# Kernel optimization log

Hardware: AMD Instinct MI355X
Metric: run time of the kernel (lower is better)

Reference implementation:

```python
import math
import jax, jax.numpy as jnp
import numpy as np

B, A, U, S, E, HYP, H = 16384, 32, 64, 2048, 32, 64, 4
ATTEND_REG_COEF = 1e-3


def setup_inputs() -> dict:
    key = jax.random.key(0)
    ks = jax.random.split(key, 12)
    sc = 0.05
    return {
        "agent_qs": jax.random.normal(ks[0], (B, A), jnp.float32),
        "states": jax.random.normal(ks[1], (B, S), jnp.float32),
        # per-head selector hypernet: Linear(S,HYP)+ReLU+Linear(HYP,E,no bias)
        "sel_w1": jax.random.normal(ks[2], (H, S, HYP), jnp.float32) * sc,
        "sel_b1": jax.random.normal(ks[3], (H, HYP), jnp.float32) * sc,
        "sel_w2": jax.random.normal(ks[4], (H, HYP, E), jnp.float32) * sc,
        # per-head key extractor: Linear(U,E,no bias)
        "key_w": jax.random.normal(ks[5], (H, U, E), jnp.float32) * sc,
        # V net: Linear(S,E)+ReLU+Linear(E,1)
        "v_w1": jax.random.normal(ks[6], (S, E), jnp.float32) * sc,
        "v_b1": jax.random.normal(ks[7], (E,), jnp.float32) * sc,
        "v_w2": jax.random.normal(ks[8], (E, 1), jnp.float32) * sc,
        "v_b2": jax.random.normal(ks[9], (1,), jnp.float32) * sc,
    }


def reference(agent_qs, states, sel_w1, sel_b1, sel_w2, key_w, v_w1, v_b1, v_w2, v_b2):
    # nonlinear=False, weighted_head=False, state_bias=True (defaults used here)
    unit_states = states[:, : A * U].reshape(-1, A, U)  # [B, A, U]

    # per-head selectors: [B, H, E]
    h1 = jax.nn.relu(jnp.einsum("bs,hsk->bhk", states, sel_w1) + sel_b1[None])
    selectors = jnp.einsum("bhk,hke->bhe", h1, sel_w2)

    # per-head, per-agent keys: [B, H, A, E]
    keys = jnp.einsum("bau,hue->bhae", unit_states, key_w)

    # attention logits [B, H, A] (matches selector @ stacked-keys in torch)
    logits = jnp.einsum("bhe,bhae->bha", selectors, keys)
    weights = jax.nn.softmax(logits / math.sqrt(E), axis=-1)  # [B, H, A]

    head_attend = jnp.sum(weights, axis=1)  # [B, A]

    v = jax.nn.relu(states @ v_w1 + v_b1) @ v_w2 + v_b2  # [B, 1]

    # coef * sum over heads of mean(logits_h ** 2)
    attend_mag_regs = ATTEND_REG_COEF * jnp.sum(jnp.mean(logits ** 2, axis=(0, 2)))

    # per-head entropy: -(p * log(p + 1e-8)).sum(agents).mean(batch) -> [H]
    head_entropies = -jnp.mean(
        jnp.sum(weights * jnp.log(weights + 1e-8), axis=-1), axis=0
    )

    return head_attend, v, attend_mag_regs, head_entropies
```

## Files before the change

### kernel.cpp

```cpp
#include <hip/hip_runtime.h>
#include <hip/hip_bf16.h>

#define B_N 16384
#define A_N 32
#define U_N 64
#define S_N 2048
#define E_N 32
#define HYP_N 64
#define H_N 4
#define NPAD 320
#define NREAL 288

#define WS_SB    0
#define WS_WT    67108864
#define WS_C1    (67108864 + 1310720)
#define WS_KWT   (WS_C1 + 9437184)
#define WS_PMAG  (WS_KWT + 32768)
#define WS_PENT  (WS_PMAG + 65536)

#define OUT_V   (B_N * A_N)
#define OUT_MAG (OUT_V + B_N)
#define OUT_ENT (OUT_MAG + 1)

typedef __attribute__((ext_vector_type(8))) short bf16x8_t;
typedef __attribute__((ext_vector_type(4))) float floatx4_t;

#define AS1(p) ((const __attribute__((address_space(1))) void*)(p))
#define AS3(p) ((__attribute__((address_space(3))) void*)(p))

__device__ __forceinline__ unsigned short f2b(float f) {
    union { float f; unsigned u; } v; v.f = f;
    unsigned r = v.u + 0x7FFFu + ((v.u >> 16) & 1u);
    return (unsigned short)(r >> 16);
}
__device__ __forceinline__ float b2f(unsigned x) {
    union { unsigned u; float f; } v; v.u = x << 16; return v.f;
}

__global__ __launch_bounds__(256) void cvt_states_kernel(
        const float* __restrict__ in, unsigned short* __restrict__ outp) {
    size_t i = ((size_t)blockIdx.x * 256 + threadIdx.x) * 8;
    float4 a = *(const float4*)(in + i);
    float4 b = *(const float4*)(in + i + 4);
    uint4 o;
    o.x = (unsigned)f2b(a.x) | ((unsigned)f2b(a.y) << 16);
    o.y = (unsigned)f2b(a.z) | ((unsigned)f2b(a.w) << 16);
    o.z = (unsigned)f2b(b.x) | ((unsigned)f2b(b.y) << 16);
    o.w = (unsigned)f2b(b.z) | ((unsigned)f2b(b.w) << 16);
    *(uint4*)(outp + i) = o;
}

__global__ __launch_bounds__(256) void pack_w_kernel(
        const float* __restrict__ sel_w1, const float* __restrict__ v_w1,
        const float* __restrict__ key_w,
        unsigned short* __restrict__ Wt, float* __restrict__ kwT) {
    int idx = blockIdx.x * 256 + threadIdx.x;
    if (idx < NPAD * S_N) {
        int n = idx >> 11;
        int k = idx & 2047;
        float val = 0.0f;
        if (n < 256) {
            int h = n >> 6, kk = n & 63;
            val = sel_w1[((size_t)h * S_N + k) * HYP_N + kk];
        } else if (n < NREAL) {
            val = v_w1[(size_t)k * E_N + (n - 256)];
        }
        Wt[idx] = f2b(val);
    } else if (idx < NPAD * S_N + H_N * E_N * U_N) {
        int j = idx - NPAD * S_N;
        int h = j >> 11, e = (j >> 6) & 31, u = j & 63;
        kwT[j] = key_w[((size_t)h * U_N + u) * E_N + e];
    }
}

#define GM_BM 128
#define GM_BN 64
#define GM_BK 64

__global__ __launch_bounds__(256) void gemm1_mfma_kernel(
        const unsigned short* __restrict__ Sb, const unsigned short* __restrict__ Wt,
        const float* __restrict__ sel_b1, const float* __restrict__ v_b1,
        unsigned short* __restrict__ C1) {
    __shared__ __align__(16) unsigned short Asm[GM_BM * GM_BK];
    __shared__ __align__(16) unsigned short Bsm[GM_BN * GM_BK];

    const int t = threadIdx.x;
    const int lane = t & 63;
    const int w = t >> 6;
    const int m0 = blockIdx.y * GM_BM;
    const int n0 = blockIdx.x * GM_BN;
    const int mw = (w >> 1) * 64;
    const int nw = (w & 1) * 32;

    floatx4_t acc[4][2] = {};

    for (int k0 = 0; k0 < S_N; k0 += GM_BK) {
        __syncthreads();
#pragma unroll
        for (int i = 0; i < 4; ++i) {
            int p = i * 256 + t;
            int r = p >> 3;
            int cl = (p & 7) ^ (r & 7);
            const unsigned short* g = Sb + (size_t)(m0 + r) * S_N + k0 + cl * 8;
            __builtin_amdgcn_global_load_lds(AS1(g), AS3(Asm + p * 8), 16, 0, 0);
        }
#pragma unroll
        for (int i = 0; i < 2; ++i) {
            int p = i * 256 + t;
            int n = p >> 3;
            int cl = (p & 7) ^ (n & 7);
            const unsigned short* g = Wt + (size_t)(n0 + n) * S_N + k0 + cl * 8;
            __builtin_amdgcn_global_load_lds(AS1(g), AS3(Bsm + p * 8), 16, 0, 0);
        }
        __syncthreads();

#pragma unroll
        for (int s = 0; s < 2; ++s) {
            const int c = s * 4 + (lane >> 4);
            bf16x8_t bfr[2];
#pragma unroll
            for (int nt = 0; nt < 2; ++nt) {
                int n = nw + nt * 16 + (lane & 15);
                int ph = c ^ (n & 7);
                bfr[nt] = *(const bf16x8_t*)(Bsm + n * 64 + ph * 8);
            }
#pragma unroll
            for (int mt = 0; mt < 4; ++mt) {
                int r = mw + mt * 16 + (lane & 15);
                int ph = c ^ (r & 7);
                bf16x8_t afr = *(const bf16x8_t*)(Asm + r * 64 + ph * 8);
#pragma unroll
                for (int nt = 0; nt < 2; ++nt)
                    acc[mt][nt] = __builtin_amdgcn_mfma_f32_16x16x32_bf16(
                        afr, bfr[nt], acc[mt][nt], 0, 0, 0);
            }
        }
    }

#pragma unroll
    for (int nt = 0; nt < 2; ++nt) {
        int n = n0 + nw + nt * 16 + (lane & 15);
        if (n >= NREAL) continue;
        float bias = (n < 256) ? sel_b1[n] : v_b1[n - 256];
#pragma unroll
        for (int mt = 0; mt < 4; ++mt) {
            int rbase = m0 + mw + mt * 16 + (lane >> 4) * 4;
#pragma unroll
            for (int rg = 0; rg < 4; ++rg) {
                float v = acc[mt][nt][rg] + bias;
                C1[(size_t)(rbase + rg) * NREAL + n] = f2b(v > 0.0f ? v : 0.0f);
            }
        }
    }
}

__global__ __launch_bounds__(256) void epilogue2_kernel(
        const unsigned short* __restrict__ Sb, const unsigned short* __restrict__ C1,
        const float* __restrict__ sel_w2, const float* __restrict__ kwT,
        const float* __restrict__ v_w2, const float* __restrict__ v_b2,
        float* __restrict__ out, float* __restrict__ pmag, float* __restrict__ pent) {
    __shared__ float us[4][A_N * 65];
    __shared__ float h1s[4][NREAL];
    __shared__ float sel_s[4][H_N * E_N];
    __shared__ float ts[4][H_N * U_N];

    const int t = threadIdx.x;
    const int w = t >> 6;
    const int lane = t & 63;
    const int b = blockIdx.x * 4 + w;

#pragma unroll
    for (int i = 0; i < 4; ++i) {
        int c = i * 64 + lane;
        uint4 v = *(const uint4*)(Sb + (size_t)b * S_N + c * 8);
        int a = c >> 3, u0 = (c & 7) * 8;
        float* d = &us[w][a * 65 + u0];
        d[0] = b2f(v.x & 0xffff); d[1] = b2f(v.x >> 16);
        d[2] = b2f(v.y & 0xffff); d[3] = b2f(v.y >> 16);
        d[4] = b2f(v.z & 0xffff); d[5] = b2f(v.z >> 16);
        d[6] = b2f(v.w & 0xffff); d[7] = b2f(v.w >> 16);
    }
    if (lane < 36) {
        uint4 v = *(const uint4*)(C1 + (size_t)b * NREAL + lane * 8);
        float* d = &h1s[w][lane * 8];
        d[0] = b2f(v.x & 0xffff); d[1] = b2f(v.x >> 16);
        d[2] = b2f(v.y & 0xffff); d[3] = b2f(v.y >> 16);
        d[4] = b2f(v.z & 0xffff); d[5] = b2f(v.z >> 16);
        d[6] = b2f(v.w & 0xffff); d[7] = b2f(v.w >> 16);
    }
    __syncthreads();

#pragma unroll
    for (int l = 0; l < 2; ++l) {
        int idx = l * 64 + lane, h = idx >> 5, e = idx & 31;
        const float* hh = &h1s[w][h * HYP_N];
        const float* w2 = sel_w2 + (size_t)h * HYP_N * E_N + e;
        float s = 0.0f;
#pragma unroll
        for (int k = 0; k < HYP_N; ++k) s = fmaf(hh[k], w2[(size_t)k * E_N], s);
        sel_s[w][idx] = s;
    }
    __syncthreads();

#pragma unroll
    for (int l = 0; l < 4; ++l) {
        int idx = l * 64 + lane, h = idx >> 6, u = idx & 63;
        const float* sh = &sel_s[w][h * E_N];
        const float* kw = kwT + (size_t)h * E_N * U_N + u;
        float s = 0.0f;
#pragma unroll
        for (int e = 0; e < E_N; ++e) s = fmaf(sh[e], kw[(size_t)e * U_N], s);
        ts[w][idx] = s;
    }
    __syncthreads();

    float wgt[2];
    float mag = 0.0f;
#pragma unroll
    for (int l = 0; l < 2; ++l) {
        int idx = l * 64 + lane, h = idx >> 5, a = idx & 31;
        const float* ua = &us[w][a * 65];
        const float* th = &ts[w][h * U_N];
        float lg = 0.0f;
#pragma unroll
        for (int u = 0; u < U_N; ++u) lg = fmaf(ua[u], th[u], lg);
        mag += lg * lg;

        float x = lg * 0.17677669529663687f;
        float m = x;
#pragma unroll
        for (int o = 16; o > 0; o >>= 1) m = fmaxf(m, __shfl_xor(m, o, 32));
        float p = expf(x - m);
        float den = p;
#pragma unroll
        for (int o = 16; o > 0; o >>= 1) den += __shfl_xor(den, o, 32);
        float wv = p / den;
        wgt[l] = wv;

        float ent = wv * logf(wv + 1e-8f);
#pragma unroll
        for (int o = 16; o > 0; o >>= 1) ent += __shfl_xor(ent, o, 32);
        if (a == 0) pent[(size_t)h * B_N + b] = ent;
    }

#pragma unroll
    for (int o = 32; o > 0; o >>= 1) mag += __shfl_xor(mag, o, 64);
    if (lane == 0) pmag[b] = mag;

    float partial = wgt[0] + wgt[1];
    partial += __shfl_xor(partial, 32, 64);
    if (lane < 32) out[(size_t)b * A_N + lane] = partial;

    if (lane < 32) {
        float p = h1s[w][256 + lane] * v_w2[lane];
#pragma unroll
        for (int o = 16; o > 0; o >>= 1) p += __shfl_xor(p, o, 32);
        if (lane == 0) out[OUT_V + b] = p + v_b2[0];
    }
}

__global__ __launch_bounds__(256) void finalize_kernel(
        const float* __restrict__ pmag, const float* __restrict__ pent,
        float* __restrict__ out) {
    int which = blockIdx.x;
    const float* src = (which == 0) ? pmag : (pent + (size_t)(which - 1) * B_N);
    float s = 0.0f;
    for (int i = threadIdx.x; i < B_N; i += 256) s += src[i];
#pragma unroll
    for (int o = 32; o > 0; o >>= 1) s += __shfl_xor(s, o, 64);
    __shared__ float red[4];
    if ((threadIdx.x & 63) == 0) red[threadIdx.x >> 6] = s;
    __syncthreads();
    if (threadIdx.x == 0) {
        float tot = red[0] + red[1] + red[2] + red[3];
        if (which == 0) out[OUT_MAG] = 1e-3f * tot / (float)(B_N * A_N);
        else out[OUT_ENT + which - 1] = -tot / (float)B_N;
    }
}

extern "C" void kernel_launch(void* const* d_in, const int* in_sizes, int n_in,
                              void* d_out, int out_size, void* d_ws, size_t ws_size,
                              hipStream_t stream) {
    const float* states = (const float*)d_in[1];
    const float* sel_w1 = (const float*)d_in[2];
    const float* sel_b1 = (const float*)d_in[3];
    const float* sel_w2 = (const float*)d_in[4];
    const float* key_w  = (const float*)d_in[5];
    const float* v_w1   = (const float*)d_in[6];
    const float* v_b1   = (const float*)d_in[7];
    const float* v_w2   = (const float*)d_in[8];
    const float* v_b2   = (const float*)d_in[9];
    float* out = (float*)d_out;
    char* wsb  = (char*)d_ws;

    unsigned short* Sb  = (unsigned short*)(wsb + WS_SB);
    unsigned short* Wt  = (unsigned short*)(wsb + WS_WT);
    unsigned short* C1  = (unsigned short*)(wsb + WS_C1);
    float* kwT          = (float*)(wsb + WS_KWT);
    float* pmag         = (float*)(wsb + WS_PMAG);
    float* pent         = (float*)(wsb + WS_PENT);

    cvt_states_kernel<<<dim3(B_N * S_N / (256 * 8)), dim3(256), 0, stream>>>(states, Sb);
    pack_w_kernel<<<dim3((NPAD * S_N + H_N * E_N * U_N + 255) / 256), dim3(256), 0, stream>>>(
        sel_w1, v_w1, key_w, Wt, kwT);
    gemm1_mfma_kernel<<<dim3(NPAD / GM_BN, B_N / GM_BM), dim3(256), 0, stream>>>(
        Sb, Wt, sel_b1, v_b1, C1);
    epilogue2_kernel<<<dim3(B_N / 4), dim3(256), 0, stream>>>(
        Sb, C1, sel_w2, kwT, v_w2, v_b2, out, pmag, pent);
    finalize_kernel<<<dim3(5), dim3(256), 0, stream>>>(pmag, pent, out);
}
```

Measured before the change: 340.6 us.

## Fuse states fp32-to-bf16 conversion into GEMM and cover full N per block

Removes the separate states conversion kernel and its 64MB bf16 intermediate. The GEMM now loads fp32 states directly, converts them to bf16 in registers and stores them into swizzled LDS. Each block computes all 288 output columns for 64 rows, so states are read only once instead of once per N-tile, and the padding to 320 columns is dropped. The epilogue reads fp32 states directly. The trade-off is a larger LDS footprint, more accumulator registers per block, and synchronous loads of A that are no longer asynchronous LDS loads.

```diff
diff --git a/kernel.cpp b/kernel.cpp
--- a/kernel.cpp
+++ b/kernel.cpp
@@ -8,12 +8,10 @@
 #define E_N 32
 #define HYP_N 64
 #define H_N 4
-#define NPAD 320
 #define NREAL 288
 
-#define WS_SB    0
-#define WS_WT    67108864
-#define WS_C1    (67108864 + 1310720)
+#define WS_WT    0
+#define WS_C1    1179648
 #define WS_KWT   (WS_C1 + 9437184)
 #define WS_PMAG  (WS_KWT + 32768)
 #define WS_PENT  (WS_PMAG + 65536)
@@ -35,19 +33,6 @@
 }
 __device__ __forceinline__ float b2f(unsigned x) {
     union { unsigned u; float f; } v; v.u = x << 16; return v.f;
-}
-
-__global__ __launch_bounds__(256) void cvt_states_kernel(
-        const float* __restrict__ in, unsigned short* __restrict__ outp) {
-    size_t i = ((size_t)blockIdx.x * 256 + threadIdx.x) * 8;
-    float4 a = *(const float4*)(in + i);
-    float4 b = *(const float4*)(in + i + 4);
-    uint4 o;
-    o.x = (unsigned)f2b(a.x) | ((unsigned)f2b(a.y) << 16);
-    o.y = (unsigned)f2b(a.z) | ((unsigned)f2b(a.w) << 16);
-    o.z = (unsigned)f2b(b.x) | ((unsigned)f2b(b.y) << 16);
-    o.w = (unsigned)f2b(b.z) | ((unsigned)f2b(b.w) << 16);
-    *(uint4*)(outp + i) = o;
 }
 
 __global__ __launch_bounds__(256) void pack_w_kernel(
@@ -55,95 +40,103 @@
         const float* __restrict__ key_w,
         unsigned short* __restrict__ Wt, float* __restrict__ kwT) {
     int idx = blockIdx.x * 256 + threadIdx.x;
-    if (idx < NPAD * S_N) {
+    if (idx < NREAL * S_N) {
         int n = idx >> 11;
         int k = idx & 2047;
-        float val = 0.0f;
+        float val;
         if (n < 256) {
             int h = n >> 6, kk = n & 63;
             val = sel_w1[((size_t)h * S_N + k) * HYP_N + kk];
-        } else if (n < NREAL) {
+        } else {
             val = v_w1[(size_t)k * E_N + (n - 256)];
         }
         Wt[idx] = f2b(val);
-    } else if (idx < NPAD * S_N + H_N * E_N * U_N) {
-        int j = idx - NPAD * S_N;
+    } else if (idx < NREAL * S_N + H_N * E_N * U_N) {
+        int j = idx - NREAL * S_N;
         int h = j >> 11, e = (j >> 6) & 31, u = j & 63;
         kwT[j] = key_w[((size_t)h * U_N + u) * E_N + e];
     }
 }
 
-#define GM_BM 128
-#define GM_BN 64
+#define GM_BM 64
 #define GM_BK 64
 
-__global__ __launch_bounds__(256) void gemm1_mfma_kernel(
-        const unsigned short* __restrict__ Sb, const unsigned short* __restrict__ Wt,
+__global__ __launch_bounds__(256) void gemm2_kernel(
+        const float* __restrict__ states, const unsigned short* __restrict__ Wt,
         const float* __restrict__ sel_b1, const float* __restrict__ v_b1,
         unsigned short* __restrict__ C1) {
     __shared__ __align__(16) unsigned short Asm[GM_BM * GM_BK];
-    __shared__ __align__(16) unsigned short Bsm[GM_BN * GM_BK];
+    __shared__ __align__(16) unsigned short Bsm[NREAL * GM_BK];
 
     const int t = threadIdx.x;
     const int lane = t & 63;
     const int w = t >> 6;
-    const int m0 = blockIdx.y * GM_BM;
-    const int n0 = blockIdx.x * GM_BN;
-    const int mw = (w >> 1) * 64;
-    const int nw = (w & 1) * 32;
-
-    floatx4_t acc[4][2] = {};
+    const int m0 = blockIdx.x * GM_BM;
+    const int mw = (w >> 1) * 32;
+    const int nw = (w & 1) * 144;
+
+    floatx4_t acc[2][9] = {};
 
     for (int k0 = 0; k0 < S_N; k0 += GM_BK) {
         __syncthreads();
-#pragma unroll
-        for (int i = 0; i < 4; ++i) {
-            int p = i * 256 + t;
-            int r = p >> 3;
-            int cl = (p & 7) ^ (r & 7);
-            const unsigned short* g = Sb + (size_t)(m0 + r) * S_N + k0 + cl * 8;
-            __builtin_amdgcn_global_load_lds(AS1(g), AS3(Asm + p * 8), 16, 0, 0);
-        }
+
+        float4 av[2][2];
 #pragma unroll
         for (int i = 0; i < 2; ++i) {
-            int p = i * 256 + t;
-            int n = p >> 3;
-            int cl = (p & 7) ^ (n & 7);
-            const unsigned short* g = Wt + (size_t)(n0 + n) * S_N + k0 + cl * 8;
+            int p = i * 256 + t, r = p >> 3, cl = p & 7;
+            const float* g = states + (size_t)(m0 + r) * S_N + k0 + cl * 8;
+            av[i][0] = *(const float4*)g;
+            av[i][1] = *(const float4*)(g + 4);
+        }
+#pragma unroll
+        for (int i = 0; i < 9; ++i) {
+            int p = i * 256 + t, n = p >> 3, sl = p & 7;
+            int cl = sl ^ (n & 7);
+            const unsigned short* g = Wt + (size_t)n * S_N + k0 + cl * 8;
             __builtin_amdgcn_global_load_lds(AS1(g), AS3(Bsm + p * 8), 16, 0, 0);
+        }
+#pragma unroll
+        for (int i = 0; i < 2; ++i) {
+            int p = i * 256 + t, r = p >> 3, cl = p & 7;
+            int ph = cl ^ (r & 7);
+            uint4 o;
+            o.x = (unsigned)f2b(av[i][0].x) | ((unsigned)f2b(av[i][0].y) << 16);
+            o.y = (unsigned)f2b(av[i][0].z) | ((unsigned)f2b(av[i][0].w) << 16);
+            o.z = (unsigned)f2b(av[i][1].x) | ((unsigned)f2b(av[i][1].y) << 16);
+            o.w = (unsigned)f2b(av[i][1].z) | ((unsigned)f2b(av[i][1].w) << 16);
+            *(uint4*)(Asm + (size_t)(r * 8 + ph) * 8) = o;
         }
         __syncthreads();
 
 #pragma unroll
         for (int s = 0; s < 2; ++s) {
             const int c = s * 4 + (lane >> 4);
-            bf16x8_t bfr[2];
-#pragma unroll
-            for (int nt = 0; nt < 2; ++nt) {
+            bf16x8_t afr[2];
+#pragma unroll
+            for (int mt = 0; mt < 2; ++mt) {
+                int r = mw + mt * 16 + (lane & 15);
+                int ph = c ^ (r & 7);
+                afr[mt] = *(const bf16x8_t*)(Asm + r * 64 + ph * 8);
+            }
+#pragma unroll
+            for (int nt = 0; nt < 9; ++nt) {
                 int n = nw + nt * 16 + (lane & 15);
                 int ph = c ^ (n & 7);
-                bfr[nt] = *(const bf16x8_t*)(Bsm + n * 64 + ph * 8);
+                bf16x8_t bfr = *(const bf16x8_t*)(Bsm + n * 64 + ph * 8);
+                acc[0][nt] = __builtin_amdgcn_mfma_f32_16x16x32_bf16(
+                    afr[0], bfr, acc[0][nt], 0, 0, 0);
+                acc[1][nt] = __builtin_amdgcn_mfma_f32_16x16x32_bf16(
+                    afr[1], bfr, acc[1][nt], 0, 0, 0);
             }
-#pragma unroll
-            for (int mt = 0; mt < 4; ++mt) {
-                int r = mw + mt * 16 + (lane & 15);
-                int ph = c ^ (r & 7);
-                bf16x8_t afr = *(const bf16x8_t*)(Asm + r * 64 + ph * 8);
-#pragma unroll
-                for (int nt = 0; nt < 2; ++nt)
-                    acc[mt][nt] = __builtin_amdgcn_mfma_f32_16x16x32_bf16(
-                        afr, bfr[nt], acc[mt][nt], 0, 0, 0);
-            }
-        }
-    }
-
-#pragma unroll
-    for (int nt = 0; nt < 2; ++nt) {
-        int n = n0 + nw + nt * 16 + (lane & 15);
-        if (n >= NREAL) continue;
+        }
+    }
+
+#pragma unroll
+    for (int nt = 0; nt < 9; ++nt) {
+        int n = nw + nt * 16 + (lane & 15);
         float bias = (n < 256) ? sel_b1[n] : v_b1[n - 256];
 #pragma unroll
-        for (int mt = 0; mt < 4; ++mt) {
+        for (int mt = 0; mt < 2; ++mt) {
             int rbase = m0 + mw + mt * 16 + (lane >> 4) * 4;
 #pragma unroll
             for (int rg = 0; rg < 4; ++rg) {
@@ -155,7 +148,7 @@
 }
 
 __global__ __launch_bounds__(256) void epilogue2_kernel(
-        const unsigned short* __restrict__ Sb, const unsigned short* __restrict__ C1,
+        const float* __restrict__ states, const unsigned short* __restrict__ C1,
         const float* __restrict__ sel_w2, const float* __restrict__ kwT,
         const float* __restrict__ v_w2, const float* __restrict__ v_b2,
         float* __restrict__ out, float* __restrict__ pmag, float* __restrict__ pent) {
@@ -169,16 +162,16 @@
     const int lane = t & 63;
     const int b = blockIdx.x * 4 + w;
 
-#pragma unroll
-    for (int i = 0; i < 4; ++i) {
-        int c = i * 64 + lane;
-        uint4 v = *(const uint4*)(Sb + (size_t)b * S_N + c * 8);
-        int a = c >> 3, u0 = (c & 7) * 8;
-        float* d = &us[w][a * 65 + u0];
-        d[0] = b2f(v.x & 0xffff); d[1] = b2f(v.x >> 16);
-        d[2] = b2f(v.y & 0xffff); d[3] = b2f(v.y >> 16);
-        d[4] = b2f(v.z & 0xffff); d[5] = b2f(v.z >> 16);
-        d[6] = b2f(v.w & 0xffff); d[7] = b2f(v.w >> 16);
+    {
+        const float4* src = (const float4*)(states + (size_t)b * S_N);
+#pragma unroll
+        for (int i = 0; i < 8; ++i) {
+            int f = i * 64 + lane;
+            float4 v4 = src[f];
+            int a = f >> 4, u = (f & 15) << 2;
+            float* d = &us[w][a * 65 + u];
+            d[0] = v4.x; d[1] = v4.y; d[2] = v4.z; d[3] = v4.w;
+        }
     }
     if (lane < 36) {
         uint4 v = *(const uint4*)(C1 + (size_t)b * NREAL + lane * 8);
@@ -293,19 +286,17 @@
     float* out = (float*)d_out;
     char* wsb  = (char*)d_ws;
 
-    unsigned short* Sb  = (unsigned short*)(wsb + WS_SB);
     unsigned short* Wt  = (unsigned short*)(wsb + WS_WT);
     unsigned short* C1  = (unsigned short*)(wsb + WS_C1);
     float* kwT          = (float*)(wsb + WS_KWT);
     float* pmag         = (float*)(wsb + WS_PMAG);
     float* pent         = (float*)(wsb + WS_PENT);
 
-    cvt_states_kernel<<<dim3(B_N * S_N / (256 * 8)), dim3(256), 0, stream>>>(states, Sb);
-    pack_w_kernel<<<dim3((NPAD * S_N + H_N * E_N * U_N + 255) / 256), dim3(256), 0, stream>>>(
+    pack_w_kernel<<<dim3((NREAL * S_N + H_N * E_N * U_N + 255) / 256), dim3(256), 0, stream>>>(
         sel_w1, v_w1, key_w, Wt, kwT);
-    gemm1_mfma_kernel<<<dim3(NPAD / GM_BN, B_N / GM_BM), dim3(256), 0, stream>>>(
-        Sb, Wt, sel_b1, v_b1, C1);
+    gemm2_kernel<<<dim3(B_N / GM_BM), dim3(256), 0, stream>>>(
+        states, Wt, sel_b1, v_b1, C1);
     epilogue2_kernel<<<dim3(B_N / 4), dim3(256), 0, stream>>>(
-        Sb, C1, sel_w2, kwT, v_w2, v_b2, out, pmag, pent);
+        states, C1, sel_w2, kwT, v_w2, v_b2, out, pmag, pent);
     finalize_kernel<<<dim3(5), dim3(256), 0, stream>>>(pmag, pent, out);
 }
```

After: 318.9 us. 1.07x faster.
